# Performance work log

Hardware: AMD Instinct MI355X
Metric: run time of the kernel (lower is better)

The kernel has to match this reference:

```python
import jax, jax.numpy as jnp
import numpy as np

N_NODES = 100000
N_EDGES = 1200000
IN_DIM = 64
HID = 64
N_GRAPHS = 512
N_CLASSES = 1
LN_EPS = 1e-5
NORM_EPS = 1e-12


def _layer_norm(x, g, b):
    mu = x.mean(-1, keepdims=True)
    var = ((x - mu) ** 2).mean(-1, keepdims=True)
    return (x - mu) * jax.lax.rsqrt(var + LN_EPS) * g + b


def setup_inputs() -> dict:
    key = jax.random.key(0)
    ks = jax.random.split(key, 20)
    h = jax.random.normal(ks[0], (N_NODES, IN_DIM), jnp.float32)
    src = jax.random.randint(ks[1], (N_EDGES,), 0, N_NODES)
    dst = jax.random.randint(ks[2], (N_EDGES,), 0, N_NODES)
    graph_ids = jnp.sort(jax.random.randint(ks[3], (N_NODES,), 0, N_GRAPHS))
    s1 = 1.0 / np.sqrt(IN_DIM)
    s2 = 1.0 / np.sqrt(HID)
    s3 = 1.0 / np.sqrt(2 * HID)
    return {
        "h": h, "src": src, "dst": dst, "graph_ids": graph_ids,
        "W1": jax.random.normal(ks[4], (IN_DIM, HID), jnp.float32) * s1,
        "b1": jnp.zeros((HID,), jnp.float32),
        "W2": jax.random.normal(ks[5], (HID, HID), jnp.float32) * s2,
        "b2": jnp.zeros((HID,), jnp.float32),
        "g1": jnp.ones((HID,), jnp.float32), "be1": jnp.zeros((HID,), jnp.float32),
        "g2": jnp.ones((HID,), jnp.float32), "be2": jnp.zeros((HID,), jnp.float32),
        "g3": jnp.ones((HID,), jnp.float32), "be3": jnp.zeros((HID,), jnp.float32),
        "g4": jnp.ones((HID,), jnp.float32), "be4": jnp.zeros((HID,), jnp.float32),
        "Wc1": jax.random.normal(ks[6], (2 * HID, HID), jnp.float32) * s3,
        "bc1": jnp.zeros((HID,), jnp.float32),
        "Wc2": jax.random.normal(ks[7], (HID, HID), jnp.float32) * s2,
        "bc2": jnp.zeros((HID,), jnp.float32),
        "Wc3": jax.random.normal(ks[8], (HID, N_CLASSES), jnp.float32) * s2,
        "bc3": jnp.zeros((N_CLASSES,), jnp.float32),
    }


def reference(h, src, dst, graph_ids, W1, b1, W2, b2, g1, be1, g2, be2,
              g3, be3, g4, be4, Wc1, bc1, Wc2, bc2, Wc3, bc3):
    N = N_NODES
    ones_e = jnp.ones((src.shape[0],), jnp.float32)
    # DGL GraphConv norm='both': symmetric degree normalization (clamp 0 -> 1)
    deg_out = jnp.clip(jax.ops.segment_sum(ones_e, src, num_segments=N), 1.0)
    deg_in = jnp.clip(jax.ops.segment_sum(ones_e, dst, num_segments=N), 1.0)
    ns = (deg_out ** -0.5)[:, None]
    nd = (deg_in ** -0.5)[:, None]

    def conv(x, W, b):
        msg = (x * ns)[src]                                  # [E, d] gather
        agg = jax.ops.segment_sum(msg, dst, num_segments=N)  # [N, d] scatter-add
        return (agg * nd) @ W + b

    h1 = jax.nn.relu(_layer_norm(conv(h, W1, b1), g1, be1))
    h1 = jax.nn.relu(_layer_norm(conv(h1, W2, b2), g2, be2))

    # per-graph mean / max pooling (dgl.mean_nodes / dgl.max_nodes)
    ssum = jax.ops.segment_sum(h1, graph_ids, num_segments=N_GRAPHS)
    cnt = jnp.clip(jax.ops.segment_sum(jnp.ones((N,), jnp.float32), graph_ids,
                                       num_segments=N_GRAPHS), 1.0)
    hg = ssum / cnt[:, None]
    hg_max = jax.ops.segment_max(h1, graph_ids, num_segments=N_GRAPHS)

    def l2norm(x):  # F.normalize(p=2, dim=1)
        n = jnp.sqrt((x * x).sum(-1, keepdims=True))
        return x / jnp.maximum(n, NORM_EPS)

    hg = jnp.concatenate([l2norm(hg), l2norm(hg_max)], axis=1)  # [G, 2*HID]
    out = jax.nn.relu(_layer_norm(hg @ Wc1 + bc1, g3, be3))
    out = jax.nn.relu(_layer_norm(out @ Wc2 + bc2, g4, be4))
    return out @ Wc3 + bc3
```

## Files before the change

### kernel.cpp

```cpp
#include <hip/hip_runtime.h>
#include <math.h>

#define HID 64
#define LN_EPS 1e-5f
#define NORM_EPS 1e-12f
#define CHUNK 1024
#define CONV_BLOCKS 2048

typedef _Float16 half4v __attribute__((ext_vector_type(4)));

__device__ __forceinline__ float wave_sum64(float v) {
#pragma unroll
    for (int o = 32; o > 0; o >>= 1) v += __shfl_xor(v, o, 64);
    return v;
}

__device__ __forceinline__ int lower_bound_dev(const int* __restrict__ a, int n, int key) {
    int lo = 0, hi = n;
    while (lo < hi) {
        int mid = (lo + hi) >> 1;
        if (a[mid] < key) lo = mid + 1; else hi = mid;
    }
    return lo;
}

__global__ __launch_bounds__(256) void count_kernel(const int* __restrict__ src,
                                                    const int* __restrict__ dst,
                                                    int* __restrict__ cnt_out,
                                                    int* __restrict__ cnt_in,
                                                    int E) {
    int e0 = (blockIdx.x * 256 + threadIdx.x) * 4;
    if (e0 + 3 < E) {
        int4 s4 = *reinterpret_cast<const int4*>(src + e0);
        int4 d4 = *reinterpret_cast<const int4*>(dst + e0);
        atomicAdd(&cnt_out[s4.x], 1); atomicAdd(&cnt_out[s4.y], 1);
        atomicAdd(&cnt_out[s4.z], 1); atomicAdd(&cnt_out[s4.w], 1);
        atomicAdd(&cnt_in[d4.x], 1);  atomicAdd(&cnt_in[d4.y], 1);
        atomicAdd(&cnt_in[d4.z], 1);  atomicAdd(&cnt_in[d4.w], 1);
    } else {
        for (int e = e0; e < E; ++e) {
            atomicAdd(&cnt_out[src[e]], 1);
            atomicAdd(&cnt_in[dst[e]], 1);
        }
    }
}

__global__ __launch_bounds__(256) void scan1_kernel(const int* __restrict__ cnt_in,
                                                    const int* __restrict__ cnt_out,
                                                    float* __restrict__ ns,
                                                    float* __restrict__ nd,
                                                    int* __restrict__ cs,
                                                    int* __restrict__ partials,
                                                    int N) {
    __shared__ int wsum[4];
    int t = threadIdx.x;
    int lane = t & 63, wave = t >> 6;
    int base = blockIdx.x * CHUNK + t * 4;
    int v0 = (base + 0 < N) ? cnt_in[base + 0] : 0;
    int v1 = (base + 1 < N) ? cnt_in[base + 1] : 0;
    int v2 = (base + 2 < N) ? cnt_in[base + 2] : 0;
    int v3 = (base + 3 < N) ? cnt_in[base + 3] : 0;

    if (base + 3 < N) {
        int4 co = *reinterpret_cast<const int4*>(cnt_out + base);
        float4 nsv = make_float4(rsqrtf((float)max(co.x, 1)), rsqrtf((float)max(co.y, 1)),
                                 rsqrtf((float)max(co.z, 1)), rsqrtf((float)max(co.w, 1)));
        float4 ndv = make_float4(rsqrtf((float)max(v0, 1)), rsqrtf((float)max(v1, 1)),
                                 rsqrtf((float)max(v2, 1)), rsqrtf((float)max(v3, 1)));
        *reinterpret_cast<float4*>(ns + base) = nsv;
        *reinterpret_cast<float4*>(nd + base) = ndv;
    } else {
        for (int i = base; i < N; ++i) {
            ns[i] = rsqrtf((float)max(cnt_out[i], 1));
            nd[i] = rsqrtf((float)max(cnt_in[i], 1));
        }
    }

    int tsum = v0 + v1 + v2 + v3;
    int x = tsum;
#pragma unroll
    for (int off = 1; off < 64; off <<= 1) {
        int y = __shfl_up(x, off, 64);
        if (lane >= off) x += y;
    }
    if (lane == 63) wsum[wave] = x;
    __syncthreads();
    int waveoff = 0;
    for (int w = 0; w < wave; ++w) waveoff += wsum[w];
    int off0 = waveoff + x - tsum;
    if (base + 0 < N) cs[base + 0] = off0;
    if (base + 1 < N) cs[base + 1] = off0 + v0;
    if (base + 2 < N) cs[base + 2] = off0 + v0 + v1;
    if (base + 3 < N) cs[base + 3] = off0 + v0 + v1 + v2;
    if (t == 255) partials[blockIdx.x] = waveoff + x;
}

__global__ __launch_bounds__(256) void scan2_kernel(int* __restrict__ partials, int nch) {
    __shared__ int wsum[4];
    int t = threadIdx.x;
    int lane = t & 63, wave = t >> 6;
    int base = t * 4;
    int v0 = (base + 0 < nch) ? partials[base + 0] : 0;
    int v1 = (base + 1 < nch) ? partials[base + 1] : 0;
    int v2 = (base + 2 < nch) ? partials[base + 2] : 0;
    int v3 = (base + 3 < nch) ? partials[base + 3] : 0;
    int tsum = v0 + v1 + v2 + v3;
    int x = tsum;
#pragma unroll
    for (int off = 1; off < 64; off <<= 1) {
        int y = __shfl_up(x, off, 64);
        if (lane >= off) x += y;
    }
    if (lane == 63) wsum[wave] = x;
    __syncthreads();
    int waveoff = 0;
    for (int w = 0; w < wave; ++w) waveoff += wsum[w];
    int off0 = waveoff + x - tsum;
    if (base + 0 < nch) partials[base + 0] = off0;
    if (base + 1 < nch) partials[base + 1] = off0 + v0;
    if (base + 2 < nch) partials[base + 2] = off0 + v0 + v1;
    if (base + 3 < nch) partials[base + 3] = off0 + v0 + v1 + v2;
}

__global__ __launch_bounds__(256) void scan3_kernel(int* __restrict__ cs,
                                                    const int* __restrict__ partials,
                                                    int* __restrict__ cursor,
                                                    int N, int E) {
    int n = blockIdx.x * 256 + threadIdx.x;
    if (n < N) {
        int v = cs[n] + partials[n / CHUNK];
        cs[n] = v;
        cursor[n] = v;
    }
    if (n == 0) cs[N] = E;
}

__global__ __launch_bounds__(256) void prescale_kernel(const float* __restrict__ x,
                                                       const float* __restrict__ ns,
                                                       _Float16* __restrict__ xs,
                                                       int total) {
    int i = (blockIdx.x * 256 + threadIdx.x) * 4;
    if (i >= total) return;
    float w = ns[i >> 6];
    float4 v = *reinterpret_cast<const float4*>(x + i);
    half4v o;
    o.x = (_Float16)(v.x * w);
    o.y = (_Float16)(v.y * w);
    o.z = (_Float16)(v.z * w);
    o.w = (_Float16)(v.w * w);
    *reinterpret_cast<half4v*>(xs + i) = o;
}

__global__ __launch_bounds__(256) void fill_kernel(const int* __restrict__ src,
                                                   const int* __restrict__ dst,
                                                   int* __restrict__ cursor,
                                                   int* __restrict__ eidx,
                                                   int E) {
    int e0 = (blockIdx.x * 256 + threadIdx.x) * 4;
    if (e0 + 3 < E) {
        int4 s4 = *reinterpret_cast<const int4*>(src + e0);
        int4 d4 = *reinterpret_cast<const int4*>(dst + e0);
        int p0 = atomicAdd(&cursor[d4.x], 1);
        int p1 = atomicAdd(&cursor[d4.y], 1);
        int p2 = atomicAdd(&cursor[d4.z], 1);
        int p3 = atomicAdd(&cursor[d4.w], 1);
        eidx[p0] = s4.x;
        eidx[p1] = s4.y;
        eidx[p2] = s4.z;
        eidx[p3] = s4.w;
    } else {
        for (int e = e0; e < E; ++e) {
            int p = atomicAdd(&cursor[dst[e]], 1);
            eidx[p] = src[e];
        }
    }
}

template <int MODE>
__global__ __launch_bounds__(256, 8) void conv_kernel(const _Float16* __restrict__ xs,
                                                      const int* __restrict__ eidx,
                                                      const int* __restrict__ cs,
                                                      const float* __restrict__ nd,
                                                      const float* __restrict__ ns,
                                                      const float* __restrict__ W,
                                                      const float* __restrict__ b,
                                                      const float* __restrict__ gam,
                                                      const float* __restrict__ bet,
                                                      void* __restrict__ outp,
                                                      int N) {
    __shared__ float Ws[HID * HID];
    int tid = threadIdx.x;
#pragma unroll
    for (int i = tid; i < HID * HID / 4; i += 256) {
        reinterpret_cast<float4*>(Ws)[i] = reinterpret_cast<const float4*>(W)[i];
    }
    __syncthreads();
    int wave = tid >> 6;
    int lane = tid & 63;
    float bl = b[lane], gl = gam[lane], bel = bet[lane];

    for (int n = blockIdx.x * 4 + wave; n < N; n += CONV_BLOCKS * 4) {
        int beg = cs[n], end = cs[n + 1];
        float acc = 0.0f;
        int e = beg;
        for (; e + 4 <= end; e += 4) {
            int s0 = eidx[e + 0];
            int s1 = eidx[e + 1];
            int s2 = eidx[e + 2];
            int s3 = eidx[e + 3];
            float v0 = (float)xs[(size_t)s0 * HID + lane];
            float v1 = (float)xs[(size_t)s1 * HID + lane];
            float v2 = (float)xs[(size_t)s2 * HID + lane];
            float v3 = (float)xs[(size_t)s3 * HID + lane];
            acc += (v0 + v1) + (v2 + v3);
        }
        for (; e < end; ++e) {
            acc += (float)xs[(size_t)eidx[e] * HID + lane];
        }
        float t = acc * nd[n];

        float y = bl;
#pragma unroll 8
        for (int k = 0; k < HID; ++k) {
            y = fmaf(__shfl(t, k, 64), Ws[k * HID + lane], y);
        }
        float mu = wave_sum64(y) * (1.0f / HID);
        float d = y - mu;
        float var = wave_sum64(d * d) * (1.0f / HID);
        float o = d * rsqrtf(var + LN_EPS) * gl + bel;
        o = fmaxf(o, 0.0f);
        if (MODE == 1) {
            ((_Float16*)outp)[(size_t)n * HID + lane] = (_Float16)(o * ns[n]);
        } else {
            ((float*)outp)[(size_t)n * HID + lane] = o;
        }
    }
}

__global__ __launch_bounds__(256) void pool_kernel(const float* __restrict__ h1,
                                                   const int* __restrict__ gid,
                                                   float* __restrict__ gsum,
                                                   float* __restrict__ gmaxf,
                                                   float* __restrict__ gcnt,
                                                   int N) {
    __shared__ float psum[4][HID];
    __shared__ float pmax[4][HID];
    __shared__ int se[2];
    int g = blockIdx.x;
    int tid = threadIdx.x;
    if (tid == 0) se[0] = lower_bound_dev(gid, N, g);
    if (tid == 64) se[1] = lower_bound_dev(gid, N, g + 1);
    __syncthreads();
    int s = se[0], e = se[1];
    int wave = tid >> 6, lane = tid & 63;
    float sum = 0.0f, mx = 0.0f;
    for (int r = s + wave; r < e; r += 4) {
        float v = h1[(size_t)r * HID + lane];
        sum += v;
        mx = fmaxf(mx, v);
    }
    psum[wave][lane] = sum;
    pmax[wave][lane] = mx;
    __syncthreads();
    if (tid < HID) {
        float ts = psum[0][tid] + psum[1][tid] + psum[2][tid] + psum[3][tid];
        float tm = fmaxf(fmaxf(pmax[0][tid], pmax[1][tid]), fmaxf(pmax[2][tid], pmax[3][tid]));
        gsum[(size_t)g * HID + tid] = ts;
        gmaxf[(size_t)g * HID + tid] = tm;
        if (tid == 0) gcnt[g] = (float)(e - s);
    }
}

__global__ __launch_bounds__(64) void head_kernel(const float* __restrict__ gsum,
                                                  const float* __restrict__ gmaxf,
                                                  const float* __restrict__ gcnt,
                                                  const float* __restrict__ Wc1,
                                                  const float* __restrict__ bc1,
                                                  const float* __restrict__ g3,
                                                  const float* __restrict__ be3,
                                                  const float* __restrict__ Wc2,
                                                  const float* __restrict__ bc2,
                                                  const float* __restrict__ g4,
                                                  const float* __restrict__ be4,
                                                  const float* __restrict__ Wc3,
                                                  const float* __restrict__ bc3,
                                                  float* __restrict__ out) {
    __shared__ float hg[2 * HID];
    __shared__ float t1[HID];
    int g = blockIdx.x;
    int lane = threadIdx.x;

    float cnt = fmaxf(gcnt[g], 1.0f);
    float mean = gsum[(size_t)g * HID + lane] / cnt;
    float mx = gmaxf[(size_t)g * HID + lane];

    float s1 = sqrtf(wave_sum64(mean * mean));
    float a = mean / fmaxf(s1, NORM_EPS);
    float s2 = sqrtf(wave_sum64(mx * mx));
    float bmx = mx / fmaxf(s2, NORM_EPS);

    hg[lane] = a;
    hg[HID + lane] = bmx;
    __syncthreads();

    float y = bc1[lane];
#pragma unroll 8
    for (int k = 0; k < 2 * HID; ++k) {
        y = fmaf(hg[k], Wc1[k * HID + lane], y);
    }
    float mu = wave_sum64(y) * (1.0f / HID);
    float d = y - mu;
    float var = wave_sum64(d * d) * (1.0f / HID);
    float o = d * rsqrtf(var + LN_EPS) * g3[lane] + be3[lane];
    o = fmaxf(o, 0.0f);
    t1[lane] = o;
    __syncthreads();

    float y2 = bc2[lane];
#pragma unroll 8
    for (int k = 0; k < HID; ++k) {
        y2 = fmaf(t1[k], Wc2[k * HID + lane], y2);
    }
    mu = wave_sum64(y2) * (1.0f / HID);
    d = y2 - mu;
    var = wave_sum64(d * d) * (1.0f / HID);
    o = d * rsqrtf(var + LN_EPS) * g4[lane] + be4[lane];
    o = fmaxf(o, 0.0f);

    float v = o * Wc3[lane];
    v = wave_sum64(v);
    if (lane == 0) out[g] = v + bc3[0];
}

extern "C" void kernel_launch(void* const* d_in, const int* in_sizes, int n_in,
                              void* d_out, int out_size, void* d_ws, size_t ws_size,
                              hipStream_t stream) {
    const float* h   = (const float*)d_in[0];
    const int*   src = (const int*)d_in[1];
    const int*   dst = (const int*)d_in[2];
    const int*   gid = (const int*)d_in[3];
    const float* W1  = (const float*)d_in[4];
    const float* b1  = (const float*)d_in[5];
    const float* W2  = (const float*)d_in[6];
    const float* b2  = (const float*)d_in[7];
    const float* g1  = (const float*)d_in[8];
    const float* be1 = (const float*)d_in[9];
    const float* g2  = (const float*)d_in[10];
    const float* be2 = (const float*)d_in[11];
    const float* g3  = (const float*)d_in[12];
    const float* be3 = (const float*)d_in[13];
    const float* g4  = (const float*)d_in[14];
    const float* be4 = (const float*)d_in[15];
    const float* Wc1 = (const float*)d_in[16];
    const float* bc1 = (const float*)d_in[17];
    const float* Wc2 = (const float*)d_in[18];
    const float* bc2 = (const float*)d_in[19];
    const float* Wc3 = (const float*)d_in[20];
    const float* bc3 = (const float*)d_in[21];
    float* out = (float*)d_out;

    const int N = in_sizes[0] / HID;
    const int E = in_sizes[1];
    const int G = out_size;

    char* ws = (char*)d_ws;
    _Float16* xs1 = (_Float16*)ws;
    _Float16* xs2 = xs1 + (size_t)N * HID;
    float* h2     = (float*)(xs2 + (size_t)N * HID);
    int*   eidx   = (int*)(h2 + (size_t)N * HID);
    float* ns     = (float*)(eidx + E);
    float* nd     = ns + N;
    int*   cnt_out= (int*)(nd + N);
    int*   cnt_in = cnt_out + N;
    int*   cs     = cnt_in + N;
    int*   partials = cs + N + 4;
    float* gsum   = (float*)(partials + 1024);
    float* gmaxf  = gsum + (size_t)G * HID;
    float* gcnt   = gmaxf + (size_t)G * HID;

    const int nch = (N + CHUNK - 1) / CHUNK;
    const int E4 = (E + 3) / 4;
    const int total = N * HID;

    hipMemsetAsync(cnt_out, 0, sizeof(int) * (size_t)2 * N, stream);

    count_kernel<<<(E4 + 255) / 256, 256, 0, stream>>>(src, dst, cnt_out, cnt_in, E);
    scan1_kernel<<<nch, 256, 0, stream>>>(cnt_in, cnt_out, ns, nd, cs, partials, N);
    scan2_kernel<<<1, 256, 0, stream>>>(partials, nch);
    scan3_kernel<<<(N + 255) / 256, 256, 0, stream>>>(cs, partials, cnt_out, N, E);
    prescale_kernel<<<(total / 4 + 255) / 256, 256, 0, stream>>>(h, ns, xs1, total);
    fill_kernel<<<(E4 + 255) / 256, 256, 0, stream>>>(src, dst, cnt_out, eidx, E);

    conv_kernel<1><<<CONV_BLOCKS, 256, 0, stream>>>(xs1, eidx, cs, nd, ns, W1, b1, g1, be1, xs2, N);
    conv_kernel<0><<<CONV_BLOCKS, 256, 0, stream>>>(xs2, eidx, cs, nd, ns, W2, b2, g2, be2, h2, N);

    pool_kernel<<<G, 256, 0, stream>>>(h2, gid, gsum, gmaxf, gcnt, N);

    head_kernel<<<G, 64, 0, stream>>>(gsum, gmaxf, gcnt, Wc1, bc1, g3, be3,
                                      Wc2, bc2, g4, be4, Wc3, bc3, out);
}
```

Baseline: 577.2 us.

## Gather 8 neighbors per wave with 16-byte loads, store final features as fp16

The conv gather is restructured so each wave processes 8 edges at once. Each group of 8 lanes loads a full 128-byte fp16 row as half8 vectors, and the partial sums are then reduced with cross-lane xor shuffles before the matvec. The second conv now writes its output in fp16 instead of fp32, which halves the write and pool read traffic at some precision cost. fill_kernel also uses nontemporal stores for the edge index scatter.

```diff
diff --git a/kernel.cpp b/kernel.cpp
--- a/kernel.cpp
+++ b/kernel.cpp
@@ -8,6 +8,7 @@
 #define CONV_BLOCKS 2048
 
 typedef _Float16 half4v __attribute__((ext_vector_type(4)));
+typedef _Float16 half8v __attribute__((ext_vector_type(8)));
 
 __device__ __forceinline__ float wave_sum64(float v) {
 #pragma unroll
@@ -164,10 +165,10 @@
         int p1 = atomicAdd(&cursor[d4.y], 1);
         int p2 = atomicAdd(&cursor[d4.z], 1);
         int p3 = atomicAdd(&cursor[d4.w], 1);
-        eidx[p0] = s4.x;
-        eidx[p1] = s4.y;
-        eidx[p2] = s4.z;
-        eidx[p3] = s4.w;
+        __builtin_nontemporal_store(s4.x, &eidx[p0]);
+        __builtin_nontemporal_store(s4.y, &eidx[p1]);
+        __builtin_nontemporal_store(s4.z, &eidx[p2]);
+        __builtin_nontemporal_store(s4.w, &eidx[p3]);
     } else {
         for (int e = e0; e < E; ++e) {
             int p = atomicAdd(&cursor[dst[e]], 1);
@@ -186,7 +187,7 @@
                                                       const float* __restrict__ b,
                                                       const float* __restrict__ gam,
                                                       const float* __restrict__ bet,
-                                                      void* __restrict__ outp,
+                                                      _Float16* __restrict__ outp,
                                                       int N) {
     __shared__ float Ws[HID * HID];
     int tid = threadIdx.x;
@@ -197,32 +198,60 @@
     __syncthreads();
     int wave = tid >> 6;
     int lane = tid & 63;
+    int g  = lane >> 3;
+    int sl = lane & 7;
     float bl = b[lane], gl = gam[lane], bel = bet[lane];
 
     for (int n = blockIdx.x * 4 + wave; n < N; n += CONV_BLOCKS * 4) {
         int beg = cs[n], end = cs[n + 1];
-        float acc = 0.0f;
-        int e = beg;
-        for (; e + 4 <= end; e += 4) {
-            int s0 = eidx[e + 0];
-            int s1 = eidx[e + 1];
-            int s2 = eidx[e + 2];
-            int s3 = eidx[e + 3];
-            float v0 = (float)xs[(size_t)s0 * HID + lane];
-            float v1 = (float)xs[(size_t)s1 * HID + lane];
-            float v2 = (float)xs[(size_t)s2 * HID + lane];
-            float v3 = (float)xs[(size_t)s3 * HID + lane];
-            acc += (v0 + v1) + (v2 + v3);
-        }
-        for (; e < end; ++e) {
-            acc += (float)xs[(size_t)eidx[e] * HID + lane];
-        }
-        float t = acc * nd[n];
+        float a0 = 0, a1 = 0, a2 = 0, a3 = 0, a4 = 0, a5 = 0, a6 = 0, a7 = 0;
+        int base = beg;
+        for (; base + 16 <= end; base += 16) {
+            int sA = eidx[base + g];
+            int sB = eidx[base + 8 + g];
+            half8v vA = *reinterpret_cast<const half8v*>(xs + (size_t)sA * HID + sl * 8);
+            half8v vB = *reinterpret_cast<const half8v*>(xs + (size_t)sB * HID + sl * 8);
+            a0 += (float)vA[0] + (float)vB[0];
+            a1 += (float)vA[1] + (float)vB[1];
+            a2 += (float)vA[2] + (float)vB[2];
+            a3 += (float)vA[3] + (float)vB[3];
+            a4 += (float)vA[4] + (float)vB[4];
+            a5 += (float)vA[5] + (float)vB[5];
+            a6 += (float)vA[6] + (float)vB[6];
+            a7 += (float)vA[7] + (float)vB[7];
+        }
+        for (; base < end; base += 8) {
+            int e = base + g;
+            if (e < end) {
+                int s = eidx[e];
+                half8v v = *reinterpret_cast<const half8v*>(xs + (size_t)s * HID + sl * 8);
+                a0 += (float)v[0]; a1 += (float)v[1]; a2 += (float)v[2]; a3 += (float)v[3];
+                a4 += (float)v[4]; a5 += (float)v[5]; a6 += (float)v[6]; a7 += (float)v[7];
+            }
+        }
+#pragma unroll
+        for (int o = 8; o <= 32; o <<= 1) {
+            a0 += __shfl_xor(a0, o, 64); a1 += __shfl_xor(a1, o, 64);
+            a2 += __shfl_xor(a2, o, 64); a3 += __shfl_xor(a3, o, 64);
+            a4 += __shfl_xor(a4, o, 64); a5 += __shfl_xor(a5, o, 64);
+            a6 += __shfl_xor(a6, o, 64); a7 += __shfl_xor(a7, o, 64);
+        }
+        float ndv = nd[n];
+        a0 *= ndv; a1 *= ndv; a2 *= ndv; a3 *= ndv;
+        a4 *= ndv; a5 *= ndv; a6 *= ndv; a7 *= ndv;
 
         float y = bl;
-#pragma unroll 8
-        for (int k = 0; k < HID; ++k) {
-            y = fmaf(__shfl(t, k, 64), Ws[k * HID + lane], y);
+#pragma unroll 4
+        for (int ko = 0; ko < 8; ++ko) {
+            const float* wrow = Ws + ko * 8 * HID + lane;
+            y = fmaf(__shfl(a0, ko, 64), wrow[0 * HID], y);
+            y = fmaf(__shfl(a1, ko, 64), wrow[1 * HID], y);
+            y = fmaf(__shfl(a2, ko, 64), wrow[2 * HID], y);
+            y = fmaf(__shfl(a3, ko, 64), wrow[3 * HID], y);
+            y = fmaf(__shfl(a4, ko, 64), wrow[4 * HID], y);
+            y = fmaf(__shfl(a5, ko, 64), wrow[5 * HID], y);
+            y = fmaf(__shfl(a6, ko, 64), wrow[6 * HID], y);
+            y = fmaf(__shfl(a7, ko, 64), wrow[7 * HID], y);
         }
         float mu = wave_sum64(y) * (1.0f / HID);
         float d = y - mu;
@@ -230,14 +259,14 @@
         float o = d * rsqrtf(var + LN_EPS) * gl + bel;
         o = fmaxf(o, 0.0f);
         if (MODE == 1) {
-            ((_Float16*)outp)[(size_t)n * HID + lane] = (_Float16)(o * ns[n]);
+            outp[(size_t)n * HID + lane] = (_Float16)(o * ns[n]);
         } else {
-            ((float*)outp)[(size_t)n * HID + lane] = o;
-        }
-    }
-}
-
-__global__ __launch_bounds__(256) void pool_kernel(const float* __restrict__ h1,
+            outp[(size_t)n * HID + lane] = (_Float16)o;
+        }
+    }
+}
+
+__global__ __launch_bounds__(256) void pool_kernel(const _Float16* __restrict__ h1,
                                                    const int* __restrict__ gid,
                                                    float* __restrict__ gsum,
                                                    float* __restrict__ gmaxf,
@@ -255,7 +284,7 @@
     int wave = tid >> 6, lane = tid & 63;
     float sum = 0.0f, mx = 0.0f;
     for (int r = s + wave; r < e; r += 4) {
-        float v = h1[(size_t)r * HID + lane];
+        float v = (float)h1[(size_t)r * HID + lane];
         sum += v;
         mx = fmaxf(mx, v);
     }
@@ -366,7 +395,7 @@
     char* ws = (char*)d_ws;
     _Float16* xs1 = (_Float16*)ws;
     _Float16* xs2 = xs1 + (size_t)N * HID;
-    float* h2     = (float*)(xs2 + (size_t)N * HID);
+    _Float16* h2  = xs2 + (size_t)N * HID;
     int*   eidx   = (int*)(h2 + (size_t)N * HID);
     float* ns     = (float*)(eidx + E);
     float* nd     = ns + N;
@@ -392,7 +421,7 @@
     fill_kernel<<<(E4 + 255) / 256, 256, 0, stream>>>(src, dst, cnt_out, eidx, E);
 
     conv_kernel<1><<<CONV_BLOCKS, 256, 0, stream>>>(xs1, eidx, cs, nd, ns, W1, b1, g1, be1, xs2, N);
-    conv_kernel<0><<<CONV_BLOCKS, 256, 0, stream>>>(xs2, eidx, cs, nd, ns, W2, b2, g2, be2, h2, N);
+    conv_kernel<2><<<CONV_BLOCKS, 256, 0, stream>>>(xs2, eidx, cs, nd, ns, W2, b2, g2, be2, h2, N);
 
     pool_kernel<<<G, 256, 0, stream>>>(h2, gid, gsum, gmaxf, gcnt, N);
 
```

Measured after the change: 616.4 us. +6.8%, slower.

## Build CSR via two-level bucket sort and store final activations in fp16

Applied to the files above, without the earlier changes.

Replaces the per-node global atomic fill of the CSR edge list with a two-pass bucket sort. Edges are first scattered into buckets of 256 destination nodes using one global cursor per bucket, then each bucket is sorted locally with shared-memory atomics. This is meant to improve write locality and cut global atomic contention, at the cost of an extra staging buffer and one more pass. It also stores the second conv output in fp16 to halve pool-kernel traffic, which loses some precision.

```diff
diff --git a/kernel.cpp b/kernel.cpp
--- a/kernel.cpp
+++ b/kernel.cpp
@@ -6,6 +6,7 @@
 #define NORM_EPS 1e-12f
 #define CHUNK 1024
 #define CONV_BLOCKS 2048
+#define BSHIFT 8
 
 typedef _Float16 half4v __attribute__((ext_vector_type(4)));
 
@@ -124,13 +125,13 @@
 
 __global__ __launch_bounds__(256) void scan3_kernel(int* __restrict__ cs,
                                                     const int* __restrict__ partials,
-                                                    int* __restrict__ cursor,
+                                                    int* __restrict__ bcur,
                                                     int N, int E) {
     int n = blockIdx.x * 256 + threadIdx.x;
     if (n < N) {
         int v = cs[n] + partials[n / CHUNK];
         cs[n] = v;
-        cursor[n] = v;
+        if ((n & ((1 << BSHIFT) - 1)) == 0) bcur[n >> BSHIFT] = v;
     }
     if (n == 0) cs[N] = E;
 }
@@ -151,28 +152,48 @@
     *reinterpret_cast<half4v*>(xs + i) = o;
 }
 
-__global__ __launch_bounds__(256) void fill_kernel(const int* __restrict__ src,
-                                                   const int* __restrict__ dst,
-                                                   int* __restrict__ cursor,
-                                                   int* __restrict__ eidx,
-                                                   int E) {
+__global__ __launch_bounds__(256) void bucket_scatter(const int* __restrict__ src,
+                                                      const int* __restrict__ dst,
+                                                      int* __restrict__ bcur,
+                                                      int2* __restrict__ staging,
+                                                      int E) {
     int e0 = (blockIdx.x * 256 + threadIdx.x) * 4;
     if (e0 + 3 < E) {
         int4 s4 = *reinterpret_cast<const int4*>(src + e0);
         int4 d4 = *reinterpret_cast<const int4*>(dst + e0);
-        int p0 = atomicAdd(&cursor[d4.x], 1);
-        int p1 = atomicAdd(&cursor[d4.y], 1);
-        int p2 = atomicAdd(&cursor[d4.z], 1);
-        int p3 = atomicAdd(&cursor[d4.w], 1);
-        eidx[p0] = s4.x;
-        eidx[p1] = s4.y;
-        eidx[p2] = s4.z;
-        eidx[p3] = s4.w;
+        int p0 = atomicAdd(&bcur[d4.x >> BSHIFT], 1);
+        int p1 = atomicAdd(&bcur[d4.y >> BSHIFT], 1);
+        int p2 = atomicAdd(&bcur[d4.z >> BSHIFT], 1);
+        int p3 = atomicAdd(&bcur[d4.w >> BSHIFT], 1);
+        staging[p0] = make_int2(s4.x, d4.x);
+        staging[p1] = make_int2(s4.y, d4.y);
+        staging[p2] = make_int2(s4.z, d4.z);
+        staging[p3] = make_int2(s4.w, d4.w);
     } else {
         for (int e = e0; e < E; ++e) {
-            int p = atomicAdd(&cursor[dst[e]], 1);
-            eidx[p] = src[e];
-        }
+            int s = src[e], d = dst[e];
+            int p = atomicAdd(&bcur[d >> BSHIFT], 1);
+            staging[p] = make_int2(s, d);
+        }
+    }
+}
+
+__global__ __launch_bounds__(256) void bucket_sort(const int2* __restrict__ staging,
+                                                   const int* __restrict__ cs,
+                                                   int* __restrict__ eidx,
+                                                   int N) {
+    __shared__ int lcur[1 << BSHIFT];
+    int b = blockIdx.x;
+    int dbase = b << BSHIFT;
+    int dlim = min(dbase + (1 << BSHIFT), N);
+    int t = threadIdx.x;
+    if (dbase + t < dlim) lcur[t] = cs[dbase + t];
+    __syncthreads();
+    int beg = cs[dbase], end = cs[dlim];
+    for (int i = beg + t; i < end; i += 256) {
+        int2 pr = staging[i];
+        int pos = atomicAdd(&lcur[pr.y & ((1 << BSHIFT) - 1)], 1);
+        eidx[pos] = pr.x;
     }
 }
 
@@ -186,7 +207,7 @@
                                                       const float* __restrict__ b,
                                                       const float* __restrict__ gam,
                                                       const float* __restrict__ bet,
-                                                      void* __restrict__ outp,
+                                                      _Float16* __restrict__ outp,
                                                       int N) {
     __shared__ float Ws[HID * HID];
     int tid = threadIdx.x;
@@ -230,14 +251,14 @@
         float o = d * rsqrtf(var + LN_EPS) * gl + bel;
         o = fmaxf(o, 0.0f);
         if (MODE == 1) {
-            ((_Float16*)outp)[(size_t)n * HID + lane] = (_Float16)(o * ns[n]);
+            outp[(size_t)n * HID + lane] = (_Float16)(o * ns[n]);
         } else {
-            ((float*)outp)[(size_t)n * HID + lane] = o;
-        }
-    }
-}
-
-__global__ __launch_bounds__(256) void pool_kernel(const float* __restrict__ h1,
+            outp[(size_t)n * HID + lane] = (_Float16)o;
+        }
+    }
+}
+
+__global__ __launch_bounds__(256) void pool_kernel(const _Float16* __restrict__ h1,
                                                    const int* __restrict__ gid,
                                                    float* __restrict__ gsum,
                                                    float* __restrict__ gmaxf,
@@ -255,7 +276,7 @@
     int wave = tid >> 6, lane = tid & 63;
     float sum = 0.0f, mx = 0.0f;
     for (int r = s + wave; r < e; r += 4) {
-        float v = h1[(size_t)r * HID + lane];
+        float v = (float)h1[(size_t)r * HID + lane];
         sum += v;
         mx = fmaxf(mx, v);
     }
@@ -362,11 +383,13 @@
     const int N = in_sizes[0] / HID;
     const int E = in_sizes[1];
     const int G = out_size;
+    const int NB = (N + (1 << BSHIFT) - 1) >> BSHIFT;
 
     char* ws = (char*)d_ws;
-    _Float16* xs1 = (_Float16*)ws;
+    int2*  staging = (int2*)ws;
+    _Float16* xs1 = (_Float16*)(staging + E);
     _Float16* xs2 = xs1 + (size_t)N * HID;
-    float* h2     = (float*)(xs2 + (size_t)N * HID);
+    _Float16* h2  = xs2 + (size_t)N * HID;
     int*   eidx   = (int*)(h2 + (size_t)N * HID);
     float* ns     = (float*)(eidx + E);
     float* nd     = ns + N;
@@ -374,7 +397,8 @@
     int*   cnt_in = cnt_out + N;
     int*   cs     = cnt_in + N;
     int*   partials = cs + N + 4;
-    float* gsum   = (float*)(partials + 1024);
+    int*   bcur   = partials + 1024;
+    float* gsum   = (float*)(bcur + ((NB + 3) & ~3));
     float* gmaxf  = gsum + (size_t)G * HID;
     float* gcnt   = gmaxf + (size_t)G * HID;
 
@@ -387,12 +411,13 @@
     count_kernel<<<(E4 + 255) / 256, 256, 0, stream>>>(src, dst, cnt_out, cnt_in, E);
     scan1_kernel<<<nch, 256, 0, stream>>>(cnt_in, cnt_out, ns, nd, cs, partials, N);
     scan2_kernel<<<1, 256, 0, stream>>>(partials, nch);
-    scan3_kernel<<<(N + 255) / 256, 256, 0, stream>>>(cs, partials, cnt_out, N, E);
+    scan3_kernel<<<(N + 255) / 256, 256, 0, stream>>>(cs, partials, bcur, N, E);
     prescale_kernel<<<(total / 4 + 255) / 256, 256, 0, stream>>>(h, ns, xs1, total);
-    fill_kernel<<<(E4 + 255) / 256, 256, 0, stream>>>(src, dst, cnt_out, eidx, E);
+    bucket_scatter<<<(E4 + 255) / 256, 256, 0, stream>>>(src, dst, bcur, staging, E);
+    bucket_sort<<<NB, 256, 0, stream>>>(staging, cs, eidx, N);
 
     conv_kernel<1><<<CONV_BLOCKS, 256, 0, stream>>>(xs1, eidx, cs, nd, ns, W1, b1, g1, be1, xs2, N);
-    conv_kernel<0><<<CONV_BLOCKS, 256, 0, stream>>>(xs2, eidx, cs, nd, ns, W2, b2, g2, be2, h2, N);
+    conv_kernel<2><<<CONV_BLOCKS, 256, 0, stream>>>(xs2, eidx, cs, nd, ns, W2, b2, g2, be2, h2, N);
 
     pool_kernel<<<G, 256, 0, stream>>>(h2, gid, gsum, gmaxf, gcnt, N);
 
```

Measured after the change: 924.7 us. 1.6x slower.
